# Kernel optimization log

Measured on AMD Instinct MI355X. Metric: run time of the kernel, lower is better.

## Reference

```python
import jax, jax.numpy as jnp
import numpy as np

E = 1_000_000
D = 128
N = 100_000


def setup_inputs() -> dict:
    key = jax.random.key(0)
    k1, k2, k3 = jax.random.split(key, 3)
    msg = jax.random.normal(k1, (E, D), dtype=jnp.float32)
    index = jax.random.randint(k2, (E,), 0, N, dtype=jnp.int64)
    t = jax.random.uniform(k3, (E,), dtype=jnp.float32)
    return {"msg": msg, "index": index, "t": t, "dim_size": N}


def reference(msg, index, t, dim_size):
    # msg: [E, D], index: [E] in [0, dim_size), t: [E]
    num_events = t.shape[0]
    # segment-max of timestamps per node
    max_t = jax.ops.segment_max(t, index, num_segments=dim_size)  # [dim_size]
    # argmax: among events attaining the segment max, take the largest position
    pos = jnp.arange(num_events, dtype=jnp.int64)
    is_seg_max = t == max_t[index]
    masked_pos = jnp.where(is_seg_max, pos, jnp.int64(-1))
    argmax = jax.ops.segment_max(masked_pos, index, num_segments=dim_size)  # [dim_size]
    # empty segments -> sentinel num_events (matches torch fallback)
    counts = jax.ops.segment_sum(jnp.ones_like(index), index, num_segments=dim_size)
    argmax = jnp.where(counts == 0, jnp.int64(num_events), argmax)
    # gather the latest message per node; zeros for empty nodes
    valid = argmax < num_events  # [dim_size]
    safe_idx = jnp.clip(argmax, 0, num_events - 1)
    gathered = msg[safe_idx]  # [dim_size, D]
    out = jnp.where(valid[:, None], gathered, jnp.zeros((), dtype=msg.dtype))
    return out
```

## Files before the change

kernel.cpp:

```cpp
#include <hip/hip_runtime.h>
#include <hip/hip_bf16.h>


typedef float f4 __attribute__((ext_vector_type(4)));
typedef unsigned long long u64;

__global__ void la_init_keys(u64* __restrict__ keys, int n) {
    int i = blockIdx.x * blockDim.x + threadIdx.x;
    if (i < n) keys[i] = 0ull;
}

__device__ __forceinline__ unsigned la_ord(float tv) {
    unsigned ub = __float_as_uint(tv);
    return (ub & 0x80000000u) ? ~ub : (ub | 0x80000000u);
}

__device__ __forceinline__ void la_update(u64* __restrict__ keys,
                                          int node, u64 cand) {
    u64 cur = __hip_atomic_load(&keys[node], __ATOMIC_RELAXED,
                                __HIP_MEMORY_SCOPE_AGENT);
    if (cand > cur) atomicMax(&keys[node], cand);
}

__global__ void la_scan_events4(const int4* __restrict__ index4,
                                const float4* __restrict__ t4,
                                u64* __restrict__ keys,
                                int Equads) {
    int i = blockIdx.x * blockDim.x + threadIdx.x;
    if (i >= Equads) return;
    float4 tv = t4[i];
    int4   ix = index4[i];
    unsigned e0 = 4u * (unsigned)i;
    u64 k0 = ((u64)la_ord(tv.x) << 32) | (u64)(e0 + 0u);
    u64 k1 = ((u64)la_ord(tv.y) << 32) | (u64)(e0 + 1u);
    u64 k2 = ((u64)la_ord(tv.z) << 32) | (u64)(e0 + 2u);
    u64 k3 = ((u64)la_ord(tv.w) << 32) | (u64)(e0 + 3u);
    u64 c0 = __hip_atomic_load(&keys[ix.x], __ATOMIC_RELAXED, __HIP_MEMORY_SCOPE_AGENT);
    u64 c1 = __hip_atomic_load(&keys[ix.y], __ATOMIC_RELAXED, __HIP_MEMORY_SCOPE_AGENT);
    u64 c2 = __hip_atomic_load(&keys[ix.z], __ATOMIC_RELAXED, __HIP_MEMORY_SCOPE_AGENT);
    u64 c3 = __hip_atomic_load(&keys[ix.w], __ATOMIC_RELAXED, __HIP_MEMORY_SCOPE_AGENT);
    if (k0 > c0) atomicMax(&keys[ix.x], k0);
    if (k1 > c1) atomicMax(&keys[ix.y], k1);
    if (k2 > c2) atomicMax(&keys[ix.z], k2);
    if (k3 > c3) atomicMax(&keys[ix.w], k3);
}

__global__ void la_scan_tail(const int* __restrict__ index,
                             const float* __restrict__ t,
                             u64* __restrict__ keys,
                             int start, int E) {
    int i = start + blockIdx.x * blockDim.x + threadIdx.x;
    if (i < E) {
        u64 k = ((u64)la_ord(t[i]) << 32) | (unsigned)i;
        la_update(keys, index[i], k);
    }
}

template <int VEC, int SHIFT>
__global__ void la_gather_v(const u64* __restrict__ keys,
                            const f4* __restrict__ msg,
                            f4* __restrict__ out,
                            int N) {
    long long gid = (long long)blockIdx.x * blockDim.x + threadIdx.x;
    int row = (int)(gid >> SHIFT);
    int col = (int)(gid & (VEC - 1));
    if (row < N) {
        u64 key = keys[row];
        f4 v = (f4)0.0f;
        if (key != 0ull) {
            unsigned pos = (unsigned)(key & 0xFFFFFFFFull);
            v = __builtin_nontemporal_load(&msg[(long long)pos * VEC + col]);
        }
        __builtin_nontemporal_store(v, &out[(long long)row * VEC + col]);
    }
}

__global__ void la_gather_g(const u64* __restrict__ keys,
                            const f4* __restrict__ msg,
                            f4* __restrict__ out,
                            int N, int vecPerRow) {
    long long gid = (long long)blockIdx.x * blockDim.x + threadIdx.x;
    int row = (int)(gid / vecPerRow);
    int col = (int)(gid - (long long)row * vecPerRow);
    if (row < N) {
        u64 key = keys[row];
        f4 v = (f4)0.0f;
        if (key != 0ull) {
            unsigned pos = (unsigned)(key & 0xFFFFFFFFull);
            v = __builtin_nontemporal_load(&msg[(long long)pos * vecPerRow + col]);
        }
        __builtin_nontemporal_store(v, &out[(long long)row * vecPerRow + col]);
    }
}

extern "C" void kernel_launch(void* const* d_in, const int* in_sizes, int n_in,
                              void* d_out, int out_size, void* d_ws, size_t ws_size,
                              hipStream_t stream) {
    const float* msg   = (const float*)d_in[0];
    const int*   index = (const int*)d_in[1];
    const float* t     = (const float*)d_in[2];

    const int E = in_sizes[1];
    const int D = in_sizes[0] / E;
    const int N = out_size / D;
    const int vecPerRow = D / 4;

    u64* keys = (u64*)d_ws;

    {
        int threads = 256, blocks = (N + threads - 1) / threads;
        la_init_keys<<<blocks, threads, 0, stream>>>(keys, N);
    }
    {
        int Equads = E / 4;
        int threads = 256, blocks = (Equads + threads - 1) / threads;
        if (blocks > 0)
            la_scan_events4<<<blocks, threads, 0, stream>>>(
                (const int4*)index, (const float4*)t, keys, Equads);
        int tail = E - 4 * Equads;
        if (tail > 0)
            la_scan_tail<<<1, 64, 0, stream>>>(index, t, keys, 4 * Equads, E);
    }
    {
        long long total = (long long)N * vecPerRow;
        int threads = 256;
        int blocks = (int)((total + threads - 1) / threads);
        if (vecPerRow == 32)
            la_gather_v<32, 5><<<blocks, threads, 0, stream>>>(
                keys, (const f4*)msg, (f4*)d_out, N);
        else if (vecPerRow == 16)
            la_gather_v<16, 4><<<blocks, threads, 0, stream>>>(
                keys, (const f4*)msg, (f4*)d_out, N);
        else
            la_gather_g<<<blocks, threads, 0, stream>>>(
                keys, (const f4*)msg, (f4*)d_out, N, vecPerRow);
    }
}
```

Measured before the change: 625.0 us.

## Privatize per-XCD segment-max keys with workgroup-scope atomics and merge pass

Gives each XCD its own copy of the per-node key array, chosen by reading the hardware XCC_ID register. The scan now issues unconditional workgroup-scope atomic max into that private copy instead of agent-scope atomics guarded by a load check. A new merge kernel reduces the eight copies into a final key array, which the gather then reads. The aim is to avoid cross-XCD atomic coherence traffic, at the cost of 8x larger init, an extra merge pass and more workspace, and it relies on workgroup-scope atomics staying correct across CUs of one XCD.

```diff
diff --git a/kernel.cpp b/kernel.cpp
--- a/kernel.cpp
+++ b/kernel.cpp
@@ -5,8 +5,16 @@
 typedef float f4 __attribute__((ext_vector_type(4)));
 typedef unsigned long long u64;
 
-__global__ void la_init_keys(u64* __restrict__ keys, int n) {
-    int i = blockIdx.x * blockDim.x + threadIdx.x;
+#define NXCD 8
+
+__device__ __forceinline__ int la_xcc_id() {
+    unsigned v;
+    asm volatile("s_getreg_b32 %0, hwreg(HW_REG_XCC_ID)" : "=s"(v));
+    return (int)(v & (NXCD - 1));
+}
+
+__global__ void la_init_keys(u64* __restrict__ keys, long long n) {
+    long long i = (long long)blockIdx.x * blockDim.x + threadIdx.x;
     if (i < n) keys[i] = 0ull;
 }
 
@@ -15,17 +23,16 @@
     return (ub & 0x80000000u) ? ~ub : (ub | 0x80000000u);
 }
 
-__device__ __forceinline__ void la_update(u64* __restrict__ keys,
-                                          int node, u64 cand) {
-    u64 cur = __hip_atomic_load(&keys[node], __ATOMIC_RELAXED,
-                                __HIP_MEMORY_SCOPE_AGENT);
-    if (cand > cur) atomicMax(&keys[node], cand);
+__device__ __forceinline__ void la_lmax(u64* __restrict__ slot, u64 cand) {
+    __hip_atomic_fetch_max(slot, cand, __ATOMIC_RELAXED,
+                           __HIP_MEMORY_SCOPE_WORKGROUP);
 }
 
 __global__ void la_scan_events4(const int4* __restrict__ index4,
                                 const float4* __restrict__ t4,
                                 u64* __restrict__ keys,
-                                int Equads) {
+                                int Equads, int N) {
+    u64* __restrict__ my = keys + (size_t)la_xcc_id() * (size_t)N;
     int i = blockIdx.x * blockDim.x + threadIdx.x;
     if (i >= Equads) return;
     float4 tv = t4[i];
@@ -35,24 +42,35 @@
     u64 k1 = ((u64)la_ord(tv.y) << 32) | (u64)(e0 + 1u);
     u64 k2 = ((u64)la_ord(tv.z) << 32) | (u64)(e0 + 2u);
     u64 k3 = ((u64)la_ord(tv.w) << 32) | (u64)(e0 + 3u);
-    u64 c0 = __hip_atomic_load(&keys[ix.x], __ATOMIC_RELAXED, __HIP_MEMORY_SCOPE_AGENT);
-    u64 c1 = __hip_atomic_load(&keys[ix.y], __ATOMIC_RELAXED, __HIP_MEMORY_SCOPE_AGENT);
-    u64 c2 = __hip_atomic_load(&keys[ix.z], __ATOMIC_RELAXED, __HIP_MEMORY_SCOPE_AGENT);
-    u64 c3 = __hip_atomic_load(&keys[ix.w], __ATOMIC_RELAXED, __HIP_MEMORY_SCOPE_AGENT);
-    if (k0 > c0) atomicMax(&keys[ix.x], k0);
-    if (k1 > c1) atomicMax(&keys[ix.y], k1);
-    if (k2 > c2) atomicMax(&keys[ix.z], k2);
-    if (k3 > c3) atomicMax(&keys[ix.w], k3);
+    la_lmax(&my[ix.x], k0);
+    la_lmax(&my[ix.y], k1);
+    la_lmax(&my[ix.z], k2);
+    la_lmax(&my[ix.w], k3);
 }
 
 __global__ void la_scan_tail(const int* __restrict__ index,
                              const float* __restrict__ t,
                              u64* __restrict__ keys,
-                             int start, int E) {
+                             int start, int E, int N) {
+    u64* __restrict__ my = keys + (size_t)la_xcc_id() * (size_t)N;
     int i = start + blockIdx.x * blockDim.x + threadIdx.x;
     if (i < E) {
         u64 k = ((u64)la_ord(t[i]) << 32) | (unsigned)i;
-        la_update(keys, index[i], k);
+        la_lmax(&my[index[i]], k);
+    }
+}
+
+__global__ void la_merge(const u64* __restrict__ keys,
+                         u64* __restrict__ finalk, int N) {
+    int n = blockIdx.x * blockDim.x + threadIdx.x;
+    if (n < N) {
+        u64 m = keys[n];
+#pragma unroll
+        for (int c = 1; c < NXCD; ++c) {
+            u64 k = keys[(size_t)c * N + n];
+            m = (k > m) ? k : m;
+        }
+        finalk[n] = m;
     }
 }
 
@@ -105,21 +123,28 @@
     const int N = out_size / D;
     const int vecPerRow = D / 4;
 
-    u64* keys = (u64*)d_ws;
+    u64* keys   = (u64*)d_ws;
+    u64* finalk = keys + (size_t)NXCD * (size_t)N;
 
     {
-        int threads = 256, blocks = (N + threads - 1) / threads;
-        la_init_keys<<<blocks, threads, 0, stream>>>(keys, N);
+        long long total = (long long)NXCD * N;
+        int threads = 256;
+        int blocks = (int)((total + threads - 1) / threads);
+        la_init_keys<<<blocks, threads, 0, stream>>>(keys, total);
     }
     {
         int Equads = E / 4;
         int threads = 256, blocks = (Equads + threads - 1) / threads;
         if (blocks > 0)
             la_scan_events4<<<blocks, threads, 0, stream>>>(
-                (const int4*)index, (const float4*)t, keys, Equads);
+                (const int4*)index, (const float4*)t, keys, Equads, N);
         int tail = E - 4 * Equads;
         if (tail > 0)
-            la_scan_tail<<<1, 64, 0, stream>>>(index, t, keys, 4 * Equads, E);
+            la_scan_tail<<<1, 64, 0, stream>>>(index, t, keys, 4 * Equads, E, N);
+    }
+    {
+        int threads = 256, blocks = (N + threads - 1) / threads;
+        la_merge<<<blocks, threads, 0, stream>>>(keys, finalk, N);
     }
     {
         long long total = (long long)N * vecPerRow;
@@ -127,12 +152,12 @@
         int blocks = (int)((total + threads - 1) / threads);
         if (vecPerRow == 32)
             la_gather_v<32, 5><<<blocks, threads, 0, stream>>>(
-                keys, (const f4*)msg, (f4*)d_out, N);
+                finalk, (const f4*)msg, (f4*)d_out, N);
         else if (vecPerRow == 16)
             la_gather_v<16, 4><<<blocks, threads, 0, stream>>>(
-                keys, (const f4*)msg, (f4*)d_out, N);
+                finalk, (const f4*)msg, (f4*)d_out, N);
         else
             la_gather_g<<<blocks, threads, 0, stream>>>(
-                keys, (const f4*)msg, (f4*)d_out, N, vecPerRow);
+                finalk, (const f4*)msg, (f4*)d_out, N, vecPerRow);
     }
 }
```

New measurement: 611.5 us. 1.02x faster.
